# Kernel optimization log

Hardware: AMD Instinct MI355X
Metric: run time of the kernel (lower is better)

## Reference

```python
import jax, jax.numpy as jnp
import numpy as np

N, E, F_IN, EDGE_DIM = 50000, 1600000, 128, 16
H, C = 4, 32            # heads, per-head channels for conv1/conv2
C_OUT = 2               # conv3: heads=1, out_channels=2
HC = H * C              # 128 = hidden_channels * heads
NEG_SLOPE = 0.2
BN_EPS = 1e-5


def setup_inputs() -> dict:
    key = jax.random.key(0)
    ks = jax.random.split(key, 40)
    rn = lambda k, s, sc: jax.random.normal(k, s, jnp.float32) * sc
    inp = {}
    inp["x"] = rn(ks[0], (N, F_IN), 1.0)
    inp["edge_index"] = jax.random.randint(ks[1], (2, E), 0, N, dtype=jnp.int32)
    inp["edge_attr"] = rn(ks[2], (E, EDGE_DIM), 1.0)
    # GATConv layer 1 (in=F_IN -> H x C)
    inp["W1"] = rn(ks[3], (F_IN, HC), F_IN ** -0.5)
    inp["as1"] = rn(ks[4], (H, C), 0.1)
    inp["ad1"] = rn(ks[5], (H, C), 0.1)
    inp["We1"] = rn(ks[6], (EDGE_DIM, HC), EDGE_DIM ** -0.5)
    inp["ae1"] = rn(ks[7], (H, C), 0.1)
    inp["b1"] = jnp.zeros((HC,), jnp.float32)
    # BN1 (eval mode: running stats)
    inp["g1"] = jnp.ones((HC,), jnp.float32)
    inp["be1"] = jnp.zeros((HC,), jnp.float32)
    inp["rm1"] = rn(ks[8], (HC,), 0.1)
    inp["rv1"] = jnp.ones((HC,), jnp.float32)
    # GATConv layer 2 (in=HC -> H x C)
    inp["W2"] = rn(ks[9], (HC, HC), HC ** -0.5)
    inp["as2"] = rn(ks[10], (H, C), 0.1)
    inp["ad2"] = rn(ks[11], (H, C), 0.1)
    inp["We2"] = rn(ks[12], (EDGE_DIM, HC), EDGE_DIM ** -0.5)
    inp["ae2"] = rn(ks[13], (H, C), 0.1)
    inp["b2"] = jnp.zeros((HC,), jnp.float32)
    inp["g2"] = jnp.ones((HC,), jnp.float32)
    inp["be2"] = jnp.zeros((HC,), jnp.float32)
    inp["rm2"] = rn(ks[14], (HC,), 0.1)
    inp["rv2"] = jnp.ones((HC,), jnp.float32)
    inp["W3"] = rn(ks[15], (HC, C_OUT), HC ** -0.5)
    inp["as3"] = rn(ks[16], (1, C_OUT), 0.1)
    inp["ad3"] = rn(ks[17], (1, C_OUT), 0.1)
    inp["We3"] = rn(ks[18], (EDGE_DIM, C_OUT), EDGE_DIM ** -0.5)
    inp["ae3"] = rn(ks[19], (1, C_OUT), 0.1)
    inp["b3"] = jnp.zeros((C_OUT,), jnp.float32)
    return inp


def _gat_layer(x, src, dst, eattr, W, a_s, a_d, We, a_e, b, heads, ch):
    """PyG GATConv (shared src/dst linear, edge_dim, add_self_loops already applied)."""
    n = x.shape[0]
    xp = (x @ W).reshape(n, heads, ch)                      # [N,H,C]
    alpha_src = (xp * a_s).sum(-1)                          # [N,H]
    alpha_dst = (xp * a_d).sum(-1)                          # [N,H]
    ep = (eattr @ We).reshape(-1, heads, ch)                # [E,H,C]
    alpha_e = (ep * a_e).sum(-1)                            # [E,H]
    alpha = alpha_src[src] + alpha_dst[dst] + alpha_e       # [E,H]
    alpha = jax.nn.leaky_relu(alpha, NEG_SLOPE)
    # segment softmax over incoming edges of each dst node
    m = jax.ops.segment_max(alpha, dst, num_segments=n)     # every node has a self loop
    ex = jnp.exp(alpha - m[dst])
    s = jax.ops.segment_sum(ex, dst, num_segments=n)
    alpha = ex / (s[dst] + 1e-16)                           # [E,H]
    msg = xp[src] * alpha[..., None]                        # [E,H,C]
    out = jax.ops.segment_sum(msg, dst, num_segments=n)     # [N,H,C]
    return out.reshape(n, heads * ch) + b


def _bn_eval(x, g, b, rm, rv):
    return (x - rm) * (g * jax.lax.rsqrt(rv + BN_EPS)) + b


def reference(x, edge_index, edge_attr,
              W1, as1, ad1, We1, ae1, b1, g1, be1, rm1, rv1,
              W2, as2, ad2, We2, ae2, b2, g2, be2, rm2, rv2,
              W3, as3, ad3, We3, ae3, b3):
    n = x.shape[0]
    loop = jnp.arange(n, dtype=edge_index.dtype)
    src = jnp.concatenate([edge_index[0], loop])
    dst = jnp.concatenate([edge_index[1], loop])
    # self-loop edge_attr fill_value='mean' (PyG default)
    ea_mean = jnp.broadcast_to(edge_attr.mean(0), (n, edge_attr.shape[1]))
    ea = jnp.concatenate([edge_attr, ea_mean], axis=0)

    h = _gat_layer(x, src, dst, ea, W1, as1, ad1, We1, ae1, b1, H, C)
    h = jax.nn.elu(_bn_eval(h, g1, be1, rm1, rv1))
    h = _gat_layer(h, src, dst, ea, W2, as2, ad2, We2, ae2, b2, H, C)
    h = jax.nn.elu(_bn_eval(h, g2, be2, rm2, rv2))
    out = _gat_layer(h, src, dst, ea, W3, as3, ad3, We3, ae3, b3, 1, C_OUT)
    return out
```

## Files before the change

### kernel.cpp

```cpp
#include <hip/hip_runtime.h>
#include <hip/hip_fp16.h>
#include <math.h>

#define NN 50000
#define EE 1600000
#define ETOT (EE + NN)
#define NEG_SLOPE 0.2f
#define BN_EPS 1e-5f
#define FILL_BLOCKS 1024
#define NB_SCAN ((NN + 255) / 256)


static __device__ inline unsigned pkh2(float a, float b) {
  __half ha = __float2half_rn(a), hb = __float2half_rn(b);
  unsigned short ua = *(unsigned short*)&ha, ub = *(unsigned short*)&hb;
  return ((unsigned)ub << 16) | ua;
}
static __device__ inline float upkh(unsigned u, int hi) {
  unsigned short s = hi ? (unsigned short)(u >> 16) : (unsigned short)(u & 0xffff);
  __half h = *(__half*)&s;
  return __half2float(h);
}

__global__ void compute_M_k(const float* __restrict__ We1, const float* __restrict__ ae1,
                            const float* __restrict__ We2, const float* __restrict__ ae2,
                            const float* __restrict__ We3, const float* __restrict__ ae3,
                            float* __restrict__ M) {
  int t = threadIdx.x;
  if (t < 64) {
    int d = t >> 2, h = t & 3;
    float s1 = 0.f, s2 = 0.f;
    for (int c = 0; c < 32; ++c) {
      s1 += We1[d * 128 + h * 32 + c] * ae1[h * 32 + c];
      s2 += We2[d * 128 + h * 32 + c] * ae2[h * 32 + c];
    }
    M[t] = s1;
    M[64 + t] = s2;
  }
  if (t < 16) {
    M[128 + t] = We3[t * 2] * ae3[0] + We3[t * 2 + 1] * ae3[1];
  }
}

__global__ void deg_k(const int* __restrict__ dst, int* __restrict__ deg) {
  int e = blockIdx.x * blockDim.x + threadIdx.x;
  if (e < EE) atomicAdd(&deg[dst[e]], 1);
}

__global__ __launch_bounds__(256) void scan_part_k(const int* __restrict__ deg,
                                                   int* __restrict__ part) {
  int t = threadIdx.x;
  int i = blockIdx.x * 256 + t;
  int v = (i < NN) ? deg[i] + 1 : 0;
#pragma unroll
  for (int off = 32; off; off >>= 1) v += __shfl_xor(v, off, 64);
  __shared__ int s[4];
  if ((t & 63) == 0) s[t >> 6] = v;
  __syncthreads();
  if (t == 0) part[blockIdx.x] = s[0] + s[1] + s[2] + s[3];
}

__global__ __launch_bounds__(256) void scan_base_k(int* __restrict__ part) {
  __shared__ int s[256];
  int t = threadIdx.x;
  int v = (t < NB_SCAN) ? part[t] : 0;
  s[t] = v;
  __syncthreads();
  for (int off = 1; off < 256; off <<= 1) {
    int u = (t >= off) ? s[t - off] : 0;
    __syncthreads();
    s[t] += u;
    __syncthreads();
  }
  if (t < NB_SCAN) part[t] = s[t] - v;
}

__global__ __launch_bounds__(256) void scan_fill_k(const int* __restrict__ deg,
                                                   const int* __restrict__ part,
                                                   int* __restrict__ row_ofs,
                                                   int* __restrict__ cursor) {
  __shared__ int s[256];
  int t = threadIdx.x;
  int i = blockIdx.x * 256 + t;
  int v = (i < NN) ? deg[i] + 1 : 0;
  s[t] = v;
  __syncthreads();
  for (int off = 1; off < 256; off <<= 1) {
    int u = (t >= off) ? s[t - off] : 0;
    __syncthreads();
    s[t] += u;
    __syncthreads();
  }
  int excl = s[t] - v + part[blockIdx.x];
  if (i < NN) {
    row_ofs[i] = excl;
    cursor[i] = excl + 1;
  }
  if (i == NN - 1) row_ofs[NN] = ETOT;
}

__global__ __launch_bounds__(256) void fill_k(const int* __restrict__ src,
                                              const int* __restrict__ dst,
                                              const float* __restrict__ ea,
                                              const float* __restrict__ M,
                                              int* __restrict__ cursor,
                                              uint2* __restrict__ recAE1,
                                              uint2* __restrict__ recAE2,
                                              float* __restrict__ rec3,
                                              int* __restrict__ recSrc,
                                              float* __restrict__ mean_part) {
  __shared__ float sM[144];
  int t = threadIdx.x;
  if (t < 144) sM[t] = M[t];
  __syncthreads();
  float macc[16];
#pragma unroll
  for (int d = 0; d < 16; ++d) macc[d] = 0.f;

  for (int e = blockIdx.x * 256 + t; e < EE; e += FILL_BLOCKS * 256) {
    float v[16];
    const float4* p = (const float4*)(ea + (size_t)e * 16);
    float4 q0 = p[0], q1 = p[1], q2 = p[2], q3 = p[3];
    v[0] = q0.x; v[1] = q0.y; v[2] = q0.z; v[3] = q0.w;
    v[4] = q1.x; v[5] = q1.y; v[6] = q1.z; v[7] = q1.w;
    v[8] = q2.x; v[9] = q2.y; v[10] = q2.z; v[11] = q2.w;
    v[12] = q3.x; v[13] = q3.y; v[14] = q3.z; v[15] = q3.w;
    float a1[4], a2[4];
#pragma unroll
    for (int h = 0; h < 4; ++h) {
      float s1 = 0.f, s2 = 0.f;
#pragma unroll
      for (int d = 0; d < 16; ++d) {
        s1 += v[d] * sM[d * 4 + h];
        s2 += v[d] * sM[64 + d * 4 + h];
      }
      a1[h] = s1; a2[h] = s2;
    }
    float a3 = 0.f;
#pragma unroll
    for (int d = 0; d < 16; ++d) a3 += v[d] * sM[128 + d];
#pragma unroll
    for (int d = 0; d < 16; ++d) macc[d] += v[d];

    int dn = dst[e], sn = src[e];
    int pos = atomicAdd(&cursor[dn], 1);
    recAE1[pos] = make_uint2(pkh2(a1[0], a1[1]), pkh2(a1[2], a1[3]));
    recAE2[pos] = make_uint2(pkh2(a2[0], a2[1]), pkh2(a2[2], a2[3]));
    rec3[pos] = a3;
    recSrc[pos] = sn;
  }
#pragma unroll
  for (int d = 0; d < 16; ++d) {
#pragma unroll
    for (int off = 32; off; off >>= 1) macc[d] += __shfl_xor(macc[d], off, 64);
  }
  __shared__ float swsum[4][16];
  int w = t >> 6, l = t & 63;
  if (l == 0) {
#pragma unroll
    for (int d = 0; d < 16; ++d) swsum[w][d] = macc[d];
  }
  __syncthreads();
  if (t < 16) {
    mean_part[(size_t)blockIdx.x * 16 + t] =
        swsum[0][t] + swsum[1][t] + swsum[2][t] + swsum[3][t];
  }
}

__global__ __launch_bounds__(256) void selfloop_k(const float* __restrict__ mean_part,
                                                  const float* __restrict__ M,
                                                  float* __restrict__ alpha_sl) {
  __shared__ float s[256];
  int t = threadIdx.x;
  int d = t & 15, c = t >> 4;
  float v = 0.f;
  for (int i = c * 64; i < (c + 1) * 64; ++i) v += mean_part[(size_t)i * 16 + d];
  s[t] = v;
  __syncthreads();
  if (t < 16) {
    float sum = 0.f;
    for (int c2 = 0; c2 < 16; ++c2) sum += s[c2 * 16 + t];
    s[t] = sum / (float)EE;
  }
  __syncthreads();
  if (t < 9) {
    float r = 0.f;
    if (t < 4) {
      for (int dd = 0; dd < 16; ++dd) r += s[dd] * M[dd * 4 + t];
    } else if (t < 8) {
      int h = t - 4;
      for (int dd = 0; dd < 16; ++dd) r += s[dd] * M[64 + dd * 4 + h];
    } else {
      for (int dd = 0; dd < 16; ++dd) r += s[dd] * M[128 + dd];
    }
    alpha_sl[t] = r;
  }
}

__global__ __launch_bounds__(256) void slrec_k(const int* __restrict__ row_ofs,
                                               const float* __restrict__ asl,
                                               uint2* __restrict__ recAE1,
                                               uint2* __restrict__ recAE2,
                                               float* __restrict__ rec3,
                                               int* __restrict__ recSrc) {
  int n = blockIdx.x * 256 + threadIdx.x;
  if (n < NN) {
    int pos = row_ofs[n];
    recAE1[pos] = make_uint2(pkh2(asl[0], asl[1]), pkh2(asl[2], asl[3]));
    recAE2[pos] = make_uint2(pkh2(asl[4], asl[5]), pkh2(asl[6], asl[7]));
    rec3[pos] = asl[8];
    recSrc[pos] = n;
  }
}

__global__ __launch_bounds__(256) void gemm128a_k(const float* __restrict__ X,
                                                  const float* __restrict__ W,
                                                  const float* __restrict__ as,
                                                  const float* __restrict__ ad,
                                                  __half* __restrict__ Y,
                                                  float* __restrict__ asrc,
                                                  float* __restrict__ adst,
                                                  int nrows) {
  __shared__ float sW[128 * 64];
  __shared__ float sX[64 * 132];
  __shared__ float sas[128], sad[128];
  int t = threadIdx.x;
  int r0 = blockIdx.x * 64;
  int cb = blockIdx.y;
  if (t < 128) { sas[t] = as[t]; sad[t] = ad[t]; }
#pragma unroll
  for (int i = 0; i < 8; ++i) {
    int flat = t + i * 256;
    int k = flat >> 4, c4 = flat & 15;
    *(float4*)&sW[k * 64 + c4 * 4] = *(const float4*)&W[k * 128 + cb * 64 + c4 * 4];
  }
  int rows = nrows - r0; if (rows > 64) rows = 64;
#pragma unroll
  for (int i = 0; i < 8; ++i) {
    int flat = t + i * 256;
    int r = flat >> 5, k4 = flat & 31;
    if (r < rows)
      *(float4*)&sX[r * 132 + k4 * 4] = *(const float4*)&X[(size_t)(r0 + r) * 128 + k4 * 4];
  }
  __syncthreads();
  int cq = t & 15, rl = t >> 4;
  float4 acc[4];
#pragma unroll
  for (int i = 0; i < 4; ++i) acc[i] = make_float4(0.f, 0.f, 0.f, 0.f);

  for (int k = 0; k < 128; k += 4) {
    float4 w0 = *(float4*)&sW[(k + 0) * 64 + cq * 4];
    float4 w1 = *(float4*)&sW[(k + 1) * 64 + cq * 4];
    float4 w2 = *(float4*)&sW[(k + 2) * 64 + cq * 4];
    float4 w3 = *(float4*)&sW[(k + 3) * 64 + cq * 4];
#pragma unroll
    for (int i = 0; i < 4; ++i) {
      float4 xv = *(float4*)&sX[(rl + i * 16) * 132 + k];
      acc[i].x += xv.x * w0.x + xv.y * w1.x + xv.z * w2.x + xv.w * w3.x;
      acc[i].y += xv.x * w0.y + xv.y * w1.y + xv.z * w2.y + xv.w * w3.y;
      acc[i].z += xv.x * w0.z + xv.y * w1.z + xv.z * w2.z + xv.w * w3.z;
      acc[i].w += xv.x * w0.w + xv.y * w1.w + xv.z * w2.w + xv.w * w3.w;
    }
  }
  int h = cb * 2 + (cq >> 3);
  int col0 = cb * 64 + cq * 4;
#pragma unroll
  for (int i = 0; i < 4; ++i) {
    int r = rl + i * 16;
    if (r < rows) {
      uint2 st;
      st.x = pkh2(acc[i].x, acc[i].y);
      st.y = pkh2(acc[i].z, acc[i].w);
      *(uint2*)&Y[(size_t)(r0 + r) * 128 + col0] = st;
      float s1 = acc[i].x * sas[col0] + acc[i].y * sas[col0 + 1] +
                 acc[i].z * sas[col0 + 2] + acc[i].w * sas[col0 + 3];
      float s2 = acc[i].x * sad[col0] + acc[i].y * sad[col0 + 1] +
                 acc[i].z * sad[col0 + 2] + acc[i].w * sad[col0 + 3];
      s1 += __shfl_xor(s1, 1, 8); s1 += __shfl_xor(s1, 2, 8); s1 += __shfl_xor(s1, 4, 8);
      s2 += __shfl_xor(s2, 1, 8); s2 += __shfl_xor(s2, 2, 8); s2 += __shfl_xor(s2, 4, 8);
      if ((cq & 7) == 0) {
        asrc[(size_t)(r0 + r) * 4 + h] = s1;
        adst[(size_t)(r0 + r) * 4 + h] = s2;
      }
    }
  }
}

__global__ __launch_bounds__(128) void agg128_k(
    const int* __restrict__ row_ofs, const unsigned* __restrict__ recAE,
    const int* __restrict__ recSrc, const __half* __restrict__ xp,
    const float* __restrict__ asrc, const float* __restrict__ adst,
    const float* __restrict__ bias, const float* __restrict__ g,
    const float* __restrict__ be, const float* __restrict__ rm,
    const float* __restrict__ rv, float* __restrict__ out) {
  int n = blockIdx.x;
  int t = threadIdx.x;
  int h = t >> 5, j = t & 31;
  int e4 = t >> 4, gg = t & 15;
  int hh = gg >> 2;
  __shared__ float s_w[4 * 64];
  __shared__ int s_src[64];
  __shared__ float sf[4], sden[4];
  __shared__ float sacc[8][132];
  int beg = row_ofs[n], end = row_ofs[n + 1];
  float adn = adst[(size_t)n * 4 + h];
  float m_run = -1e30f, s_run = 0.f;
  float acc[8];
#pragma unroll
  for (int i = 0; i < 8; ++i) acc[i] = 0.f;

  for (int base = beg; base < end; base += 64) {
    int cnt = end - base; if (cnt > 64) cnt = 64;
    float a0 = -1e30f, a1 = -1e30f;
    if (j < cnt) {
      int idx = base + j;
      float ae = upkh(recAE[(size_t)idx * 2 + (h >> 1)], h & 1);
      int sj = recSrc[idx];
      if (h == 0) s_src[j] = sj;
      float a = asrc[(size_t)sj * 4 + h] + adn + ae;
      a0 = (a > 0.f) ? a : NEG_SLOPE * a;
    }
    if (j + 32 < cnt) {
      int idx = base + j + 32;
      float ae = upkh(recAE[(size_t)idx * 2 + (h >> 1)], h & 1);
      int sj = recSrc[idx];
      if (h == 0) s_src[j + 32] = sj;
      float a = asrc[(size_t)sj * 4 + h] + adn + ae;
      a1 = (a > 0.f) ? a : NEG_SLOPE * a;
    }
    float cm = fmaxf(a0, a1);
#pragma unroll
    for (int off = 16; off; off >>= 1) cm = fmaxf(cm, __shfl_xor(cm, off, 32));
    float f = 1.f;
    if (cm > m_run) { f = expf(m_run - cm); s_run *= f; m_run = cm; }
    if (j == 0) sf[h] = f;
    float ex0 = (j < cnt) ? expf(a0 - m_run) : 0.f;
    float ex1 = (j + 32 < cnt) ? expf(a1 - m_run) : 0.f;
    s_w[h * 64 + j] = ex0;
    s_w[h * 64 + j + 32] = ex1;
    float se = ex0 + ex1;
#pragma unroll
    for (int off = 16; off; off >>= 1) se += __shfl_xor(se, off, 32);
    s_run += se;
    __syncthreads();
    float ff = sf[hh];
    if (ff != 1.f) {
#pragma unroll
      for (int i = 0; i < 8; ++i) acc[i] *= ff;
    }
    for (int e2 = 0; e2 < cnt; e2 += 8) {
      int ed = e2 + e4;
      if (ed < cnt) {
        int sj = s_src[ed];
        float w = s_w[hh * 64 + ed];
        uint4 v = *(const uint4*)&xp[(size_t)sj * 128 + gg * 8];
        acc[0] += w * upkh(v.x, 0); acc[1] += w * upkh(v.x, 1);
        acc[2] += w * upkh(v.y, 0); acc[3] += w * upkh(v.y, 1);
        acc[4] += w * upkh(v.z, 0); acc[5] += w * upkh(v.z, 1);
        acc[6] += w * upkh(v.w, 0); acc[7] += w * upkh(v.w, 1);
      }
    }
    __syncthreads();
  }
  if (j == 0) sden[h] = s_run;
#pragma unroll
  for (int i = 0; i < 8; ++i) sacc[e4][gg * 8 + i] = acc[i];
  __syncthreads();
  float v = 0.f;
#pragma unroll
  for (int i = 0; i < 8; ++i) v += sacc[i][t];
  v = v / (sden[t >> 5] + 1e-16f) + bias[t];
  v = (v - rm[t]) * (g[t] * rsqrtf(rv[t] + BN_EPS)) + be[t];
  v = (v > 0.f) ? v : (expf(v) - 1.f);
  out[(size_t)n * 128 + t] = v;
}

__global__ __launch_bounds__(256) void xp3_k(const float* __restrict__ h2,
                                             const float* __restrict__ W3,
                                             const float* __restrict__ as3,
                                             const float* __restrict__ ad3,
                                             float* __restrict__ xp3,
                                             float* __restrict__ asrc3,
                                             float* __restrict__ adst3) {
  __shared__ float sW[256];
  int t = threadIdx.x;
  sW[t] = W3[t];
  __syncthreads();
  int n = blockIdx.x * 256 + t;
  if (n < NN) {
    const float4* row = (const float4*)(h2 + (size_t)n * 128);
    float y0 = 0.f, y1 = 0.f;
#pragma unroll
    for (int i = 0; i < 32; ++i) {
      float4 v = row[i];
      y0 += v.x * sW[(i * 4 + 0) * 2] + v.y * sW[(i * 4 + 1) * 2] +
            v.z * sW[(i * 4 + 2) * 2] + v.w * sW[(i * 4 + 3) * 2];
      y1 += v.x * sW[(i * 4 + 0) * 2 + 1] + v.y * sW[(i * 4 + 1) * 2 + 1] +
            v.z * sW[(i * 4 + 2) * 2 + 1] + v.w * sW[(i * 4 + 3) * 2 + 1];
    }
    xp3[n * 2] = y0;
    xp3[n * 2 + 1] = y1;
    asrc3[n] = y0 * as3[0] + y1 * as3[1];
    adst3[n] = y0 * ad3[0] + y1 * ad3[1];
  }
}

__global__ __launch_bounds__(256) void agg2_k(const int* __restrict__ row_ofs,
                                              const float* __restrict__ rec3,
                                              const int* __restrict__ recSrc,
                                              const float* __restrict__ xp3,
                                              const float* __restrict__ asrc3,
                                              const float* __restrict__ adst3,
                                              const float* __restrict__ b3,
                                              float* __restrict__ out) {
  int t = threadIdx.x;
  int w = t >> 6, l = t & 63;
  int n = blockIdx.x * 4 + w;
  if (n >= NN) return;
  int beg = row_ofs[n], end = row_ofs[n + 1];
  float adn = adst3[n];
  float m = -1e30f, s = 0.f, a0 = 0.f, a1 = 0.f;
  for (int idx = beg + l; idx < end; idx += 64) {
    float aev = rec3[idx];
    int sj = recSrc[idx];
    float a = asrc3[sj] + adn + aev;
    a = (a > 0.f) ? a : NEG_SLOPE * a;
    if (a > m) {
      float f = expf(m - a);
      s *= f; a0 *= f; a1 *= f; m = a;
    }
    float ex = expf(a - m);
    s += ex;
    a0 += ex * xp3[sj * 2];
    a1 += ex * xp3[sj * 2 + 1];
  }
  float M = m;
#pragma unroll
  for (int off = 32; off; off >>= 1) M = fmaxf(M, __shfl_xor(M, off, 64));
  float f = expf(m - M);
  s *= f; a0 *= f; a1 *= f;
#pragma unroll
  for (int off = 32; off; off >>= 1) {
    s += __shfl_xor(s, off, 64);
    a0 += __shfl_xor(a0, off, 64);
    a1 += __shfl_xor(a1, off, 64);
  }
  if (l == 0) {
    float inv = 1.f / (s + 1e-16f);
    out[n * 2] = a0 * inv + b3[0];
    out[n * 2 + 1] = a1 * inv + b3[1];
  }
}

extern "C" void kernel_launch(void* const* d_in, const int* in_sizes, int n_in,
                              void* d_out, int out_size, void* d_ws, size_t ws_size,
                              hipStream_t stream) {
  const float* x   = (const float*)d_in[0];
  const int*   ei  = (const int*)d_in[1];
  const float* ea  = (const float*)d_in[2];
  const float* W1  = (const float*)d_in[3];
  const float* as1 = (const float*)d_in[4];
  const float* ad1 = (const float*)d_in[5];
  const float* We1 = (const float*)d_in[6];
  const float* ae1 = (const float*)d_in[7];
  const float* b1  = (const float*)d_in[8];
  const float* g1  = (const float*)d_in[9];
  const float* be1 = (const float*)d_in[10];
  const float* rm1 = (const float*)d_in[11];
  const float* rv1 = (const float*)d_in[12];
  const float* W2  = (const float*)d_in[13];
  const float* as2 = (const float*)d_in[14];
  const float* ad2 = (const float*)d_in[15];
  const float* We2 = (const float*)d_in[16];
  const float* ae2 = (const float*)d_in[17];
  const float* b2  = (const float*)d_in[18];
  const float* g2  = (const float*)d_in[19];
  const float* be2 = (const float*)d_in[20];
  const float* rm2 = (const float*)d_in[21];
  const float* rv2 = (const float*)d_in[22];
  const float* W3  = (const float*)d_in[23];
  const float* as3 = (const float*)d_in[24];
  const float* ad3 = (const float*)d_in[25];
  const float* We3 = (const float*)d_in[26];
  const float* ae3 = (const float*)d_in[27];
  const float* b3  = (const float*)d_in[28];

  const int* srcA = ei;
  const int* dstA = ei + EE;

  char* p = (char*)d_ws;
  auto alloc = [&](size_t bytes) -> void* {
    void* r = (void*)p;
    p += (bytes + 255) & ~(size_t)255;
    return r;
  };
  uint2* recAE1 = (uint2*)alloc(sizeof(uint2) * (size_t)ETOT);
  uint2* recAE2 = (uint2*)alloc(sizeof(uint2) * (size_t)ETOT);
  float* rec3   = (float*)alloc(sizeof(float) * (size_t)ETOT);
  int*   recSrc = (int*)alloc(sizeof(int) * (size_t)ETOT);
  __half* xp    = (__half*)alloc(sizeof(__half) * (size_t)NN * 128);
  float* hbuf   = (float*)alloc(sizeof(float) * (size_t)NN * 128);
  float* Mbuf   = (float*)alloc(sizeof(float) * 144);
  float* meanp  = (float*)alloc(sizeof(float) * (size_t)FILL_BLOCKS * 16);
  float* asl    = (float*)alloc(sizeof(float) * 12);
  float* asrc   = (float*)alloc(sizeof(float) * (size_t)NN * 4);
  float* adst   = (float*)alloc(sizeof(float) * (size_t)NN * 4);
  float* xp3    = (float*)alloc(sizeof(float) * (size_t)NN * 2);
  float* asrc3  = (float*)alloc(sizeof(float) * (size_t)NN);
  float* adst3  = (float*)alloc(sizeof(float) * (size_t)NN);
  int* deg      = (int*)alloc(sizeof(int) * (size_t)NN);
  int* part     = (int*)alloc(sizeof(int) * 256);
  int* row_ofs  = (int*)alloc(sizeof(int) * (size_t)(NN + 1));
  int* cursor   = (int*)alloc(sizeof(int) * (size_t)NN);

  hipMemsetAsync(deg, 0, NN * sizeof(int), stream);

  compute_M_k<<<1, 64, 0, stream>>>(We1, ae1, We2, ae2, We3, ae3, Mbuf);
  deg_k<<<(EE + 255) / 256, 256, 0, stream>>>(dstA, deg);
  scan_part_k<<<NB_SCAN, 256, 0, stream>>>(deg, part);
  scan_base_k<<<1, 256, 0, stream>>>(part);
  scan_fill_k<<<NB_SCAN, 256, 0, stream>>>(deg, part, row_ofs, cursor);
  fill_k<<<FILL_BLOCKS, 256, 0, stream>>>(srcA, dstA, ea, Mbuf, cursor,
                                          recAE1, recAE2, rec3, recSrc, meanp);
  selfloop_k<<<1, 256, 0, stream>>>(meanp, Mbuf, asl);
  slrec_k<<<(NN + 255) / 256, 256, 0, stream>>>(row_ofs, asl, recAE1, recAE2, rec3, recSrc);

  gemm128a_k<<<dim3((NN + 63) / 64, 2), 256, 0, stream>>>(x, W1, as1, ad1, xp, asrc, adst, NN);
  agg128_k<<<NN, 128, 0, stream>>>(row_ofs, (const unsigned*)recAE1, recSrc, xp,
                                   asrc, adst, b1, g1, be1, rm1, rv1, hbuf);
  gemm128a_k<<<dim3((NN + 63) / 64, 2), 256, 0, stream>>>(hbuf, W2, as2, ad2, xp, asrc, adst, NN);
  agg128_k<<<NN, 128, 0, stream>>>(row_ofs, (const unsigned*)recAE2, recSrc, xp,
                                   asrc, adst, b2, g2, be2, rm2, rv2, hbuf);
  xp3_k<<<(NN + 255) / 256, 256, 0, stream>>>(hbuf, W3, as3, ad3, xp3, asrc3, adst3);
  agg2_k<<<(NN + 3) / 4, 256, 0, stream>>>(row_ofs, rec3, recSrc, xp3, asrc3, adst3,
                                           b3, (float*)d_out);
}
```

Measured before the change: 453.9 us.

## Build CSR via permutation pass and unroll aggregation gather by two

Edge-attribute logits are now computed into a dense per-edge payload, with the degree count folded into that pass. A separate atomic pass computes a permutation, and a gather kernel builds the CSR records, self-loops included, with coalesced writes. This replaces scattered multi-array writes inside the fill kernel and drops the separate degree and self-loop record kernels, at the cost of an extra payload buffer and extra passes. The aggregation loop also now issues two neighbour loads per iteration to raise memory-level parallelism.

```diff
diff --git a/kernel.cpp b/kernel.cpp
--- a/kernel.cpp
+++ b/kernel.cpp
@@ -7,7 +7,7 @@
 #define ETOT (EE + NN)
 #define NEG_SLOPE 0.2f
 #define BN_EPS 1e-5f
-#define FILL_BLOCKS 1024
+#define PAY_BLOCKS 1024
 #define NB_SCAN ((NN + 255) / 256)
 
 
@@ -42,73 +42,13 @@
   }
 }
 
-__global__ void deg_k(const int* __restrict__ dst, int* __restrict__ deg) {
-  int e = blockIdx.x * blockDim.x + threadIdx.x;
-  if (e < EE) atomicAdd(&deg[dst[e]], 1);
-}
-
-__global__ __launch_bounds__(256) void scan_part_k(const int* __restrict__ deg,
-                                                   int* __restrict__ part) {
-  int t = threadIdx.x;
-  int i = blockIdx.x * 256 + t;
-  int v = (i < NN) ? deg[i] + 1 : 0;
-#pragma unroll
-  for (int off = 32; off; off >>= 1) v += __shfl_xor(v, off, 64);
-  __shared__ int s[4];
-  if ((t & 63) == 0) s[t >> 6] = v;
-  __syncthreads();
-  if (t == 0) part[blockIdx.x] = s[0] + s[1] + s[2] + s[3];
-}
-
-__global__ __launch_bounds__(256) void scan_base_k(int* __restrict__ part) {
-  __shared__ int s[256];
-  int t = threadIdx.x;
-  int v = (t < NB_SCAN) ? part[t] : 0;
-  s[t] = v;
-  __syncthreads();
-  for (int off = 1; off < 256; off <<= 1) {
-    int u = (t >= off) ? s[t - off] : 0;
-    __syncthreads();
-    s[t] += u;
-    __syncthreads();
-  }
-  if (t < NB_SCAN) part[t] = s[t] - v;
-}
-
-__global__ __launch_bounds__(256) void scan_fill_k(const int* __restrict__ deg,
-                                                   const int* __restrict__ part,
-                                                   int* __restrict__ row_ofs,
-                                                   int* __restrict__ cursor) {
-  __shared__ int s[256];
-  int t = threadIdx.x;
-  int i = blockIdx.x * 256 + t;
-  int v = (i < NN) ? deg[i] + 1 : 0;
-  s[t] = v;
-  __syncthreads();
-  for (int off = 1; off < 256; off <<= 1) {
-    int u = (t >= off) ? s[t - off] : 0;
-    __syncthreads();
-    s[t] += u;
-    __syncthreads();
-  }
-  int excl = s[t] - v + part[blockIdx.x];
-  if (i < NN) {
-    row_ofs[i] = excl;
-    cursor[i] = excl + 1;
-  }
-  if (i == NN - 1) row_ofs[NN] = ETOT;
-}
-
-__global__ __launch_bounds__(256) void fill_k(const int* __restrict__ src,
-                                              const int* __restrict__ dst,
-                                              const float* __restrict__ ea,
-                                              const float* __restrict__ M,
-                                              int* __restrict__ cursor,
-                                              uint2* __restrict__ recAE1,
-                                              uint2* __restrict__ recAE2,
-                                              float* __restrict__ rec3,
-                                              int* __restrict__ recSrc,
-                                              float* __restrict__ mean_part) {
+__global__ __launch_bounds__(256) void payload_k(const int* __restrict__ src,
+                                                 const int* __restrict__ dst,
+                                                 const float* __restrict__ ea,
+                                                 const float* __restrict__ M,
+                                                 int* __restrict__ deg,
+                                                 float4* __restrict__ payload,
+                                                 float* __restrict__ mean_part) {
   __shared__ float sM[144];
   int t = threadIdx.x;
   if (t < 144) sM[t] = M[t];
@@ -117,7 +57,7 @@
 #pragma unroll
   for (int d = 0; d < 16; ++d) macc[d] = 0.f;
 
-  for (int e = blockIdx.x * 256 + t; e < EE; e += FILL_BLOCKS * 256) {
+  for (int e = blockIdx.x * 256 + t; e < EE; e += PAY_BLOCKS * 256) {
     float v[16];
     const float4* p = (const float4*)(ea + (size_t)e * 16);
     float4 q0 = p[0], q1 = p[1], q2 = p[2], q3 = p[3];
@@ -142,12 +82,17 @@
 #pragma unroll
     for (int d = 0; d < 16; ++d) macc[d] += v[d];
 
-    int dn = dst[e], sn = src[e];
-    int pos = atomicAdd(&cursor[dn], 1);
-    recAE1[pos] = make_uint2(pkh2(a1[0], a1[1]), pkh2(a1[2], a1[3]));
-    recAE2[pos] = make_uint2(pkh2(a2[0], a2[1]), pkh2(a2[2], a2[3]));
-    rec3[pos] = a3;
-    recSrc[pos] = sn;
+    atomicAdd(&deg[dst[e]], 1);
+    float4 r0, r1;
+    r0.x = __uint_as_float(pkh2(a1[0], a1[1]));
+    r0.y = __uint_as_float(pkh2(a1[2], a1[3]));
+    r0.z = __uint_as_float(pkh2(a2[0], a2[1]));
+    r0.w = __uint_as_float(pkh2(a2[2], a2[3]));
+    r1.x = a3;
+    r1.y = __int_as_float(src[e]);
+    r1.z = 0.f; r1.w = 0.f;
+    payload[(size_t)e * 2] = r0;
+    payload[(size_t)e * 2 + 1] = r1;
   }
 #pragma unroll
   for (int d = 0; d < 16; ++d) {
@@ -197,19 +142,90 @@
   }
 }
 
-__global__ __launch_bounds__(256) void slrec_k(const int* __restrict__ row_ofs,
-                                               const float* __restrict__ asl,
-                                               uint2* __restrict__ recAE1,
-                                               uint2* __restrict__ recAE2,
-                                               float* __restrict__ rec3,
-                                               int* __restrict__ recSrc) {
-  int n = blockIdx.x * 256 + threadIdx.x;
-  if (n < NN) {
-    int pos = row_ofs[n];
-    recAE1[pos] = make_uint2(pkh2(asl[0], asl[1]), pkh2(asl[2], asl[3]));
-    recAE2[pos] = make_uint2(pkh2(asl[4], asl[5]), pkh2(asl[6], asl[7]));
-    rec3[pos] = asl[8];
-    recSrc[pos] = n;
+__global__ __launch_bounds__(256) void scan_part_k(const int* __restrict__ deg,
+                                                   int* __restrict__ part) {
+  int t = threadIdx.x;
+  int i = blockIdx.x * 256 + t;
+  int v = (i < NN) ? deg[i] + 1 : 0;
+#pragma unroll
+  for (int off = 32; off; off >>= 1) v += __shfl_xor(v, off, 64);
+  __shared__ int s[4];
+  if ((t & 63) == 0) s[t >> 6] = v;
+  __syncthreads();
+  if (t == 0) part[blockIdx.x] = s[0] + s[1] + s[2] + s[3];
+}
+
+__global__ __launch_bounds__(256) void scan_base_k(int* __restrict__ part) {
+  __shared__ int s[256];
+  int t = threadIdx.x;
+  int v = (t < NB_SCAN) ? part[t] : 0;
+  s[t] = v;
+  __syncthreads();
+  for (int off = 1; off < 256; off <<= 1) {
+    int u = (t >= off) ? s[t - off] : 0;
+    __syncthreads();
+    s[t] += u;
+    __syncthreads();
+  }
+  if (t < NB_SCAN) part[t] = s[t] - v;
+}
+
+__global__ __launch_bounds__(256) void scan_fill_k(const int* __restrict__ deg,
+                                                   const int* __restrict__ part,
+                                                   int* __restrict__ row_ofs,
+                                                   int* __restrict__ cursor) {
+  __shared__ int s[256];
+  int t = threadIdx.x;
+  int i = blockIdx.x * 256 + t;
+  int v = (i < NN) ? deg[i] + 1 : 0;
+  s[t] = v;
+  __syncthreads();
+  for (int off = 1; off < 256; off <<= 1) {
+    int u = (t >= off) ? s[t - off] : 0;
+    __syncthreads();
+    s[t] += u;
+    __syncthreads();
+  }
+  int excl = s[t] - v + part[blockIdx.x];
+  if (i < NN) {
+    row_ofs[i] = excl;
+    cursor[i] = excl;
+  }
+  if (i == NN - 1) row_ofs[NN] = ETOT;
+}
+
+__global__ void perm_k(const int* __restrict__ dst, int* __restrict__ cursor,
+                       int* __restrict__ perm) {
+  int e = blockIdx.x * blockDim.x + threadIdx.x;
+  if (e < ETOT) {
+    int d = (e < EE) ? dst[e] : (e - EE);
+    int pos = atomicAdd(&cursor[d], 1);
+    perm[pos] = e;
+  }
+}
+
+__global__ __launch_bounds__(256) void csrbuild_k(const int* __restrict__ perm,
+                                                  const float4* __restrict__ payload,
+                                                  const float* __restrict__ asl,
+                                                  uint2* __restrict__ recAE1,
+                                                  uint2* __restrict__ recAE2,
+                                                  float* __restrict__ rec3,
+                                                  int* __restrict__ recSrc) {
+  int i = blockIdx.x * 256 + threadIdx.x;
+  if (i >= ETOT) return;
+  int e = perm[i];
+  if (e < EE) {
+    float4 p0 = payload[(size_t)e * 2];
+    float4 p1 = payload[(size_t)e * 2 + 1];
+    recAE1[i] = make_uint2(__float_as_uint(p0.x), __float_as_uint(p0.y));
+    recAE2[i] = make_uint2(__float_as_uint(p0.z), __float_as_uint(p0.w));
+    rec3[i] = p1.x;
+    recSrc[i] = __float_as_int(p1.y);
+  } else {
+    recAE1[i] = make_uint2(pkh2(asl[0], asl[1]), pkh2(asl[2], asl[3]));
+    recAE2[i] = make_uint2(pkh2(asl[4], asl[5]), pkh2(asl[6], asl[7]));
+    rec3[i] = asl[8];
+    recSrc[i] = e - EE;
   }
 }
 
@@ -348,16 +364,30 @@
 #pragma unroll
       for (int i = 0; i < 8; ++i) acc[i] *= ff;
     }
-    for (int e2 = 0; e2 < cnt; e2 += 8) {
-      int ed = e2 + e4;
-      if (ed < cnt) {
-        int sj = s_src[ed];
-        float w = s_w[hh * 64 + ed];
-        uint4 v = *(const uint4*)&xp[(size_t)sj * 128 + gg * 8];
-        acc[0] += w * upkh(v.x, 0); acc[1] += w * upkh(v.x, 1);
-        acc[2] += w * upkh(v.y, 0); acc[3] += w * upkh(v.y, 1);
-        acc[4] += w * upkh(v.z, 0); acc[5] += w * upkh(v.z, 1);
-        acc[6] += w * upkh(v.w, 0); acc[7] += w * upkh(v.w, 1);
+    for (int e2 = 0; e2 < cnt; e2 += 16) {
+      int ed0 = e2 + e4, ed1 = e2 + e4 + 8;
+      bool b0 = ed0 < cnt, b1 = ed1 < cnt;
+      uint4 v0, v1;
+      float w0 = 0.f, w1 = 0.f;
+      if (b0) {
+        int s0 = s_src[ed0]; w0 = s_w[hh * 64 + ed0];
+        v0 = *(const uint4*)&xp[(size_t)s0 * 128 + gg * 8];
+      }
+      if (b1) {
+        int s1 = s_src[ed1]; w1 = s_w[hh * 64 + ed1];
+        v1 = *(const uint4*)&xp[(size_t)s1 * 128 + gg * 8];
+      }
+      if (b0) {
+        acc[0] += w0 * upkh(v0.x, 0); acc[1] += w0 * upkh(v0.x, 1);
+        acc[2] += w0 * upkh(v0.y, 0); acc[3] += w0 * upkh(v0.y, 1);
+        acc[4] += w0 * upkh(v0.z, 0); acc[5] += w0 * upkh(v0.z, 1);
+        acc[6] += w0 * upkh(v0.w, 0); acc[7] += w0 * upkh(v0.w, 1);
+      }
+      if (b1) {
+        acc[0] += w1 * upkh(v1.x, 0); acc[1] += w1 * upkh(v1.x, 1);
+        acc[2] += w1 * upkh(v1.y, 0); acc[3] += w1 * upkh(v1.y, 1);
+        acc[4] += w1 * upkh(v1.z, 0); acc[5] += w1 * upkh(v1.z, 1);
+        acc[6] += w1 * upkh(v1.w, 0); acc[7] += w1 * upkh(v1.w, 1);
       }
     }
     __syncthreads();
@@ -494,14 +524,16 @@
     p += (bytes + 255) & ~(size_t)255;
     return r;
   };
+  float4* payload = (float4*)alloc(32 * (size_t)EE);
   uint2* recAE1 = (uint2*)alloc(sizeof(uint2) * (size_t)ETOT);
   uint2* recAE2 = (uint2*)alloc(sizeof(uint2) * (size_t)ETOT);
   float* rec3   = (float*)alloc(sizeof(float) * (size_t)ETOT);
   int*   recSrc = (int*)alloc(sizeof(int) * (size_t)ETOT);
+  int*   perm   = (int*)alloc(sizeof(int) * (size_t)ETOT);
   __half* xp    = (__half*)alloc(sizeof(__half) * (size_t)NN * 128);
   float* hbuf   = (float*)alloc(sizeof(float) * (size_t)NN * 128);
   float* Mbuf   = (float*)alloc(sizeof(float) * 144);
-  float* meanp  = (float*)alloc(sizeof(float) * (size_t)FILL_BLOCKS * 16);
+  float* meanp  = (float*)alloc(sizeof(float) * (size_t)PAY_BLOCKS * 16);
   float* asl    = (float*)alloc(sizeof(float) * 12);
   float* asrc   = (float*)alloc(sizeof(float) * (size_t)NN * 4);
   float* adst   = (float*)alloc(sizeof(float) * (size_t)NN * 4);
@@ -516,14 +548,14 @@
   hipMemsetAsync(deg, 0, NN * sizeof(int), stream);
 
   compute_M_k<<<1, 64, 0, stream>>>(We1, ae1, We2, ae2, We3, ae3, Mbuf);
-  deg_k<<<(EE + 255) / 256, 256, 0, stream>>>(dstA, deg);
+  payload_k<<<PAY_BLOCKS, 256, 0, stream>>>(srcA, dstA, ea, Mbuf, deg, payload, meanp);
+  selfloop_k<<<1, 256, 0, stream>>>(meanp, Mbuf, asl);
   scan_part_k<<<NB_SCAN, 256, 0, stream>>>(deg, part);
   scan_base_k<<<1, 256, 0, stream>>>(part);
   scan_fill_k<<<NB_SCAN, 256, 0, stream>>>(deg, part, row_ofs, cursor);
-  fill_k<<<FILL_BLOCKS, 256, 0, stream>>>(srcA, dstA, ea, Mbuf, cursor,
-                                          recAE1, recAE2, rec3, recSrc, meanp);
-  selfloop_k<<<1, 256, 0, stream>>>(meanp, Mbuf, asl);
-  slrec_k<<<(NN + 255) / 256, 256, 0, stream>>>(row_ofs, asl, recAE1, recAE2, rec3, recSrc);
+  perm_k<<<(ETOT + 255) / 256, 256, 0, stream>>>(dstA, cursor, perm);
+  csrbuild_k<<<(ETOT + 255) / 256, 256, 0, stream>>>(perm, payload, asl,
+                                                     recAE1, recAE2, rec3, recSrc);
 
   gemm128a_k<<<dim3((NN + 63) / 64, 2), 256, 0, stream>>>(x, W1, as1, ad1, xp, asrc, adst, NN);
   agg128_k<<<NN, 128, 0, stream>>>(row_ofs, (const unsigned*)recAE1, recSrc, xp,
```

Measured after the change: 533.3 us. +17.5%, slower.
